# Optimization experiments

Hardware: AMD Instinct MI355X
Metric: run time of the kernel (lower is better)

Reference implementation:

```python
import math
import jax, jax.numpy as jnp
import numpy as np

# gpt-oss config constants (layer_idx=1 -> sliding_window disabled)
HID = 2880
N_HEADS = 64
N_KV = 8
D_HEAD = 64
GROUPS = N_HEADS // N_KV  # 8 query heads per kv head
SLIDING_WINDOW = 0        # layer_idx % 2 == 1 -> full causal attention
SM_SCALE = 1.0 / math.sqrt(D_HEAD)
EPS = 1e-5

ROPE_BASE = 150000.0
INIT_CTX = 4096
SCALING = 32.0
NTK_ALPHA = 1.0
NTK_BETA = 32.0


def _rope_cos_sin(num_tokens: int):
    """YaRN-scaled RoPE tables, fp32, positions 0..num_tokens-1 (offset=0, no cache)."""
    d_half = D_HEAD // 2
    freq = ROPE_BASE ** (np.arange(0, D_HEAD, 2, dtype=np.float64) / D_HEAD)
    concentration = 0.1 * math.log(SCALING) + 1.0
    low = d_half * math.log(INIT_CTX / (NTK_BETA * 2 * math.pi)) / math.log(ROPE_BASE)
    high = d_half * math.log(INIT_CTX / (NTK_ALPHA * 2 * math.pi)) / math.log(ROPE_BASE)
    interpolation = 1.0 / (SCALING * freq)
    extrapolation = 1.0 / freq
    ramp = (np.arange(d_half, dtype=np.float64) - low) / (high - low)
    mask = 1.0 - np.clip(ramp, 0.0, 1.0)
    inv_freq = interpolation * (1.0 - mask) + extrapolation * mask
    t = np.arange(num_tokens, dtype=np.float64)
    freqs = np.outer(t, inv_freq)  # [S, d_half]
    cos = (np.cos(freqs) * concentration).astype(np.float32)
    sin = (np.sin(freqs) * concentration).astype(np.float32)
    return jnp.asarray(cos), jnp.asarray(sin)


def _rotate(x, cos, sin):
    # x: [B, S, nh, D]; cos/sin: [S, D/2]
    c = cos[None, :, None, :]
    s = sin[None, :, None, :]
    x1, x2 = jnp.split(x, 2, axis=-1)
    return jnp.concatenate([x1 * c - x2 * s, x2 * c + x1 * s], axis=-1)


def setup_inputs() -> dict:
    key = jax.random.key(0)
    ks = jax.random.split(key, 5)
    B, S = 1, 1536
    x = jax.random.normal(ks[0], (B, S, HID), dtype=jnp.float32)
    sinks = jax.random.normal(ks[1], (N_HEADS,), dtype=jnp.float32) * 0.5
    norm_scale = jnp.ones((HID,), dtype=jnp.float32)
    qkv_dim = D_HEAD * (N_HEADS + 2 * N_KV)  # 5120
    qkv_w = jax.random.normal(ks[2], (qkv_dim, HID), dtype=jnp.float32) * 0.02
    qkv_b = jnp.zeros((qkv_dim,), dtype=jnp.float32)
    out_w = jax.random.normal(ks[3], (HID, N_HEADS * D_HEAD), dtype=jnp.float32) * 0.02
    out_b = jnp.zeros((HID,), dtype=jnp.float32)
    return {"x": x, "sinks": sinks, "norm_scale": norm_scale,
            "qkv_w": qkv_w, "qkv_b": qkv_b, "out_w": out_w, "out_b": out_b}


def reference(x, sinks, norm_scale, qkv_w, qkv_b, out_w, out_b):
    B, S, _ = x.shape
    # RMSNorm (fp32)
    t = x * jax.lax.rsqrt(jnp.mean(x * x, axis=-1, keepdims=True) + EPS) * norm_scale
    # fused QKV projection
    qkv = jnp.einsum('bsd,od->bso', t, qkv_w) + qkv_b
    q, k, v = jnp.split(qkv, [N_HEADS * D_HEAD, (N_HEADS + N_KV) * D_HEAD], axis=-1)
    q = q.reshape(B, S, N_HEADS, D_HEAD)
    k = k.reshape(B, S, N_KV, D_HEAD)
    v = v.reshape(B, S, N_KV, D_HEAD)
    # RoPE (offset = 0, no cache)
    cos, sin = _rope_cos_sin(S)
    q = _rotate(q, cos, sin)
    k = _rotate(k, cos, sin)
    # GQA: head h = g*N_KV + kv
    q = q.reshape(B, S, GROUPS, N_KV, D_HEAD)
    scores = jnp.einsum('bqgkd,bskd->bgkqs', q, k) * SM_SCALE  # [B,G,KV,S,S]
    i = jnp.arange(S)[:, None]
    j = jnp.arange(S)[None, :]
    allowed = j <= i  # causal
    if SLIDING_WINDOW > 0:
        allowed = allowed & (i - j < SLIDING_WINDOW)
    scores = jnp.where(allowed[None, None, None, :, :], scores, -1e30)
    # softmax with learned per-head sink logit in the denominator
    sink = sinks.reshape(GROUPS, N_KV)[None, :, :, None]  # [1,G,KV,1]
    m = jnp.maximum(jnp.max(scores, axis=-1), sink)       # [B,G,KV,S]
    p = jnp.exp(scores - m[..., None])
    denom = jnp.sum(p, axis=-1) + jnp.exp(sink - m)
    attn = p / denom[..., None]
    o = jnp.einsum('bgkqs,bskd->bqgkd', attn, v).reshape(B, S, N_HEADS * D_HEAD)
    y = jnp.einsum('bse,oe->bso', o, out_w) + out_b
    return x + y
```

## Files before the change

### kernel.cpp

```cpp
#include <hip/hip_runtime.h>
#include <hip/hip_bf16.h>
#include <math.h>

typedef unsigned short u16;
typedef __attribute__((ext_vector_type(8))) short bf16x8;
typedef __attribute__((ext_vector_type(4))) float f32x4;
typedef __attribute__((ext_vector_type(4))) u16 u16x4;
typedef __attribute__((ext_vector_type(8))) u16 u16x8;

#define S_LEN   1536
#define HID     2880
#define NH      64
#define NKV     8
#define DH      64
#define QKV_N   5120
#define QDIM    4096
#define KVDIM   512
#define SMSCALE 0.125f
#define EPSV    1e-5f

__device__ __forceinline__ float b2f(u16 u) {
    unsigned int v = ((unsigned int)u) << 16;
    float f; __builtin_memcpy(&f, &v, 4); return f;
}
__device__ __forceinline__ u16 f2b(float f) {
    __hip_bfloat16 h = __float2bfloat16(f);
    return *reinterpret_cast<u16*>(&h);
}
__device__ __forceinline__ void gld16(const u16* g, u16* l) {
    __builtin_amdgcn_global_load_lds(
        (const __attribute__((address_space(1))) unsigned int*)g,
        (__attribute__((address_space(3))) unsigned int*)l, 16, 0, 0);
}
#define WAIT_VM2()   __builtin_amdgcn_s_waitcnt(0xF72)
#define WAIT_VM0()   __builtin_amdgcn_s_waitcnt(0xF70)
#define WAIT_LGKM0() __builtin_amdgcn_s_waitcnt(0xC07F)

__global__ __launch_bounds__(256) void prep_kernel(
    const float* __restrict__ qkv_w, u16* __restrict__ qkv_w_bf,
    const float* __restrict__ x, const float* __restrict__ ns, u16* __restrict__ t,
    float* __restrict__ cosT, float* __restrict__ sinT,
    const float* __restrict__ out_w, u16* __restrict__ out_w_bf)
{
    __shared__ float red[4];
    const int b = blockIdx.x;
    const int tid = threadIdx.x;
    if (b < 14400) {
        int i = b * 256 + tid;
        float4 v = ((const float4*)qkv_w)[i];
        u16x4 o;
        o.x = f2b(v.x); o.y = f2b(v.y); o.z = f2b(v.z); o.w = f2b(v.w);
        ((u16x4*)qkv_w_bf)[i] = o;
    } else if (b < 15936) {
        const int s = b - 14400;
        const float* xr = x + (size_t)s * HID;
        float ss = 0.f;
        for (int i = tid; i < HID; i += 256) { float v = xr[i]; ss += v * v; }
        for (int off = 32; off > 0; off >>= 1) ss += __shfl_down(ss, off);
        if ((tid & 63) == 0) red[tid >> 6] = ss;
        __syncthreads();
        float tot = red[0] + red[1] + red[2] + red[3];
        float scale = rsqrtf(tot / (float)HID + EPSV);
        u16* tr = t + (size_t)s * HID;
        for (int i = tid; i < HID; i += 256)
            tr[i] = f2b(xr[i] * scale * ns[i]);
    } else if (b < 16128) {
        int idx = (b - 15936) * 256 + tid;
        if (idx >= S_LEN * 32) return;
        int s = idx >> 5, i = idx & 31;
        const double PI2 = 6.283185307179586476925286766559;
        double base = 150000.0;
        double freq = pow(base, (double)(2 * i) / 64.0);
        double conc = 0.1 * log(32.0) + 1.0;
        double low  = 32.0 * log(4096.0 / (32.0 * PI2)) / log(base);
        double high = 32.0 * log(4096.0 / (1.0  * PI2)) / log(base);
        double interp = 1.0 / (32.0 * freq);
        double extrap = 1.0 / freq;
        double ramp = ((double)i - low) / (high - low);
        double msk = 1.0 - fmin(fmax(ramp, 0.0), 1.0);
        double invf = interp * (1.0 - msk) + extrap * msk;
        double ang = (double)s * invf;
        cosT[idx] = (float)(cos(ang) * conc);
        sinT[idx] = (float)(sin(ang) * conc);
    } else {
        int i = (b - 16128) * 256 + tid;
        float4 v = ((const float4*)out_w)[i];
        u16x4 o;
        o.x = f2b(v.x); o.y = f2b(v.y); o.z = f2b(v.z); o.w = f2b(v.w);
        ((u16x4*)out_w_bf)[i] = o;
    }
}

__global__ __launch_bounds__(256) void conv_bf16_kernel(
    const float* __restrict__ src, u16* __restrict__ dst, int n4)
{
    int i = blockIdx.x * 256 + threadIdx.x;
    if (i >= n4) return;
    float4 v = ((const float4*)src)[i];
    u16x4 o;
    o.x = f2b(v.x); o.y = f2b(v.y); o.z = f2b(v.z); o.w = f2b(v.w);
    ((u16x4*)dst)[i] = o;
}

__global__ __launch_bounds__(512, 2) void gemm_bt_8p_kernel(
    const u16* __restrict__ A, const u16* __restrict__ B,
    u16* __restrict__ Cp, u16* __restrict__ Cp2,
    int M, int N, int K, int it0, int it1, int ntm, int ntn)
{
    extern __shared__ __align__(16) u16 smem[];
    u16* sAp = smem;
    u16* sBp = smem + 16384;

    const int tid  = threadIdx.x;
    const int wave = tid >> 6, lane = tid & 63;
    const int quad = lane >> 4, l16 = lane & 15;
    const int wm = wave >> 2, wn = wave & 3;

    const int nwg  = gridDim.x;
    const int cpx  = nwg >> 3;
    const int flat = blockIdx.x;
    const int swz  = (flat & 7) * cpx + (flat >> 3);
    const int tpz  = ntm * ntn;
    const int z    = swz / tpz;
    const int rem  = swz - z * tpz;
    const int nt   = rem / ntm;
    const int mt   = rem - nt * ntm;
    const int bm = mt * 256, bn = nt * 256;
    const int niter = z ? it1 : it0;
    const int kb    = z ? (it0 + (z - 1) * it1) * 32 : 0;
    u16* C = (z < 2) ? (Cp + (size_t)z * M * N) : Cp2;

    const int r2  = tid >> 2;
    const int ks8 = (tid & 3) * 8;
    const u16* gA0 = A + (size_t)(bm + r2) * K + kb + ks8;
    const u16* gA1 = gA0 + (size_t)128 * K;
    int brA = bn + r2;       if (brA > N - 1) brA = N - 1;
    int brB = bn + 128 + r2; if (brB > N - 1) brB = N - 1;
    const u16* gB0 = B + (size_t)brA * K + kb + ks8;
    const u16* gB1 = B + (size_t)brB * K + kb + ks8;
    const int sw = wave * 512;

    f32x4 acc[8][4];
    #pragma unroll
    for (int i = 0; i < 8; i++)
        #pragma unroll
        for (int j = 0; j < 4; j++) acc[i][j] = (f32x4){0.f, 0.f, 0.f, 0.f};

    auto stA = [&](int c, int t) {
        u16* d = sAp + c * 8192;
        const int koff = t * 32;
        gld16(gA0 + koff, d + sw);
        gld16(gA1 + koff, d + 4096 + sw);
    };
    auto stB = [&](int c, int t) {
        u16* d = sBp + c * 8192;
        const int koff = t * 32;
        gld16(gB0 + koff, d + sw);
        gld16(gB1 + koff, d + 4096 + sw);
    };

    bf16x8 bv[4];
    const int arow = wm * 128 + l16;
    const int brow = wn * 64 + l16;
    auto rdB = [&](int c) {
        const u16* p = sBp + c * 8192 + brow * 32 + quad * 8;
        #pragma unroll
        for (int nf = 0; nf < 4; nf++) bv[nf] = *(const bf16x8*)(p + nf * 16 * 32);
    };
    auto mmph = [&](int c, int mh) {
        const u16* p = sAp + c * 8192 + (arow + mh * 64) * 32 + quad * 8;
        bf16x8 av[4];
        #pragma unroll
        for (int mf = 0; mf < 4; mf++) av[mf] = *(const bf16x8*)(p + mf * 16 * 32);
        __builtin_amdgcn_s_setprio(1);
        #pragma unroll
        for (int mf = 0; mf < 4; mf++)
            #pragma unroll
            for (int nf = 0; nf < 4; nf++)
                acc[mh * 4 + mf][nf] = __builtin_amdgcn_mfma_f32_16x16x32_bf16(
                    av[mf], bv[nf], acc[mh * 4 + mf][nf], 0, 0, 0);
        __builtin_amdgcn_s_setprio(0);
    };

    stB(0, 0); stA(0, 0);

    for (int t = 0; t < niter - 1; ++t) {
        const int c = t & 1;
        stB(c ^ 1, t + 1);
        WAIT_VM2();
        __builtin_amdgcn_s_barrier();
        stA(c ^ 1, t + 1);
        rdB(c);
        mmph(c, 0);
        mmph(c, 1);
    }
    {
        const int c = (niter - 1) & 1;
        WAIT_VM0();
        __builtin_amdgcn_s_barrier();
        rdB(c);
        mmph(c, 0);
        mmph(c, 1);
    }

    #pragma unroll
    for (int im = 0; im < 8; im++) {
        const int row0 = bm + wm * 128 + im * 16 + quad * 4;
        #pragma unroll
        for (int nf = 0; nf < 4; nf++) {
            const int col = bn + wn * 64 + nf * 16 + l16;
            if (col < N) {
                #pragma unroll
                for (int r = 0; r < 4; r++)
                    C[(size_t)(row0 + r) * N + col] = f2b(acc[im][nf][r]);
            }
        }
    }
}

__global__ __launch_bounds__(256) void rope_apply_kernel(
    const u16* __restrict__ p0, const u16* __restrict__ p1, const float* __restrict__ bias,
    const float* __restrict__ cosT, const float* __restrict__ sinT,
    u16* __restrict__ q_r, u16* __restrict__ k_r, u16* __restrict__ v_r)
{
    int idx = blockIdx.x * 256 + threadIdx.x;
    if (idx >= S_LEN * 320) return;
    int s = idx / 320;
    int c = idx - s * 320;
    const u16* r0p = p0 + (size_t)s * QKV_N;
    const u16* r1p = p1 + (size_t)s * QKV_N;
    if (c < 288) {
        int hh = c >> 2, j0 = (c & 3) * 8;
        int off = hh * 64;
        u16x8 a1 = *(const u16x8*)(r0p + off + j0);
        u16x8 b1 = *(const u16x8*)(r1p + off + j0);
        u16x8 a2 = *(const u16x8*)(r0p + off + 32 + j0);
        u16x8 b2 = *(const u16x8*)(r1p + off + 32 + j0);
        float bl[8], bh[8], cc[8], sn[8];
        *(float4*)&bl[0] = *(const float4*)(bias + off + j0);
        *(float4*)&bl[4] = *(const float4*)(bias + off + j0 + 4);
        *(float4*)&bh[0] = *(const float4*)(bias + off + 32 + j0);
        *(float4*)&bh[4] = *(const float4*)(bias + off + 32 + j0 + 4);
        *(float4*)&cc[0] = *(const float4*)(cosT + s * 32 + j0);
        *(float4*)&cc[4] = *(const float4*)(cosT + s * 32 + j0 + 4);
        *(float4*)&sn[0] = *(const float4*)(sinT + s * 32 + j0);
        *(float4*)&sn[4] = *(const float4*)(sinT + s * 32 + j0 + 4);
        const float scale = (hh < 64) ? SMSCALE : 1.0f;
        u16x8 lo, hi;
        #pragma unroll
        for (int j = 0; j < 8; j++) {
            float x1 = b2f(a1[j]) + b2f(b1[j]) + bl[j];
            float x2 = b2f(a2[j]) + b2f(b2[j]) + bh[j];
            lo[j] = f2b((x1 * cc[j] - x2 * sn[j]) * scale);
            hi[j] = f2b((x2 * cc[j] + x1 * sn[j]) * scale);
        }
        if (hh < 64) {
            u16* dst = q_r + (size_t)s * QDIM + off;
            *(u16x8*)(dst + j0) = lo;
            *(u16x8*)(dst + 32 + j0) = hi;
        } else {
            u16* dst = k_r + (size_t)s * KVDIM + (hh - 64) * 64;
            *(u16x8*)(dst + j0) = lo;
            *(u16x8*)(dst + 32 + j0) = hi;
        }
    } else {
        int c2 = c - 288;
        int vh = c2 >> 2, i0 = (c2 & 3) * 16;
        int off = QDIM + KVDIM + vh * 64 + i0;
        u16x8 a0 = *(const u16x8*)(r0p + off);
        u16x8 a1 = *(const u16x8*)(r0p + off + 8);
        u16x8 b0 = *(const u16x8*)(r1p + off);
        u16x8 b1 = *(const u16x8*)(r1p + off + 8);
        float bb[16];
        *(float4*)&bb[0]  = *(const float4*)(bias + off);
        *(float4*)&bb[4]  = *(const float4*)(bias + off + 4);
        *(float4*)&bb[8]  = *(const float4*)(bias + off + 8);
        *(float4*)&bb[12] = *(const float4*)(bias + off + 12);
        u16x8 o0, o1;
        #pragma unroll
        for (int j = 0; j < 8; j++) {
            o0[j] = f2b(b2f(a0[j]) + b2f(b0[j]) + bb[j]);
            o1[j] = f2b(b2f(a1[j]) + b2f(b1[j]) + bb[8 + j]);
        }
        u16* dst = v_r + (size_t)s * KVDIM + vh * 64 + i0;
        *(u16x8*)dst = o0;
        *(u16x8*)(dst + 8) = o1;
    }
}

__global__ __launch_bounds__(256) void vt_kernel(
    const u16* __restrict__ v_r, u16* __restrict__ vt)
{
    __shared__ u16 tile[64][72];
    const int s0 = blockIdx.x * 64;
    const int kvh = blockIdx.y;
    const int tid = threadIdx.x;
    const int r = tid >> 3;
    const int c = (tid & 7) * 8;

    #pragma unroll
    for (int rr = 0; rr < 64; rr += 32) {
        uint4 vv = *(const uint4*)(v_r + (size_t)(s0 + r + rr) * KVDIM + kvh * 64 + c);
        const u16* p = (const u16*)&vv;
        #pragma unroll
        for (int j = 0; j < 8; j++) tile[c + j][r + rr] = p[j];
    }
    __syncthreads();
    #pragma unroll
    for (int rr = 0; rr < 64; rr += 32) {
        uint4 ov;
        u16* p = (u16*)&ov;
        #pragma unroll
        for (int j = 0; j < 8; j++) p[j] = tile[r + rr][c + j];
        *(uint4*)(vt + (size_t)(kvh * 64 + r + rr) * S_LEN + s0 + c) = ov;
    }
}

__global__ __launch_bounds__(256) void attn_kernel(
    const u16* __restrict__ q_r, const u16* __restrict__ k_r, const u16* __restrict__ vt,
    const float* __restrict__ sinks, u16* __restrict__ o)
{
    __shared__ __align__(16) u16 sK[2][64 * 72];
    __shared__ __align__(16) u16 sVt[2][64 * 72];
    __shared__ __align__(16) u16 sP[4 * 16 * 72];

    const int bx = blockIdx.x, h = blockIdx.y;
    const int kvh = h & 7;
    const int tid = threadIdx.x, wave = tid >> 6, lane = tid & 63;
    const int quad = lane >> 4, l16 = lane & 15;
    const int srow = tid >> 3;
    const int scol = (tid & 7) * 8;
    u16* sPw = sP + wave * 16 * 72;
    const float sinkv = sinks[h];

    uint4 kreg0, kreg1, vreg0, vreg1;
    const u16* kbase = k_r + (size_t)srow * KVDIM + kvh * 64 + scol;
    const u16* vbase = vt + (size_t)(kvh * 64 + srow) * S_LEN + scol;

    auto issue = [&](int j0) {
        kreg0 = *(const uint4*)(kbase + (size_t)j0 * KVDIM);
        kreg1 = *(const uint4*)(kbase + (size_t)(j0 + 32) * KVDIM);
        vreg0 = *(const uint4*)(vbase + j0);
        vreg1 = *(const uint4*)(vbase + (size_t)32 * S_LEN + j0);
    };
    auto lwrite = [&](int c) {
        *(uint4*)(&sK[c][srow * 72 + scol])        = kreg0;
        *(uint4*)(&sK[c][(srow + 32) * 72 + scol]) = kreg1;
        *(uint4*)(&sVt[c][srow * 72 + scol])        = vreg0;
        *(uint4*)(&sVt[c][(srow + 32) * 72 + scol]) = vreg1;
    };

    for (int phase = 0; phase < 2; ++phase) {
        const int qt = phase ? (23 - bx) : bx;
        const int q_i = qt * 64 + wave * 16 + l16;
        const u16* qp = q_r + (size_t)q_i * QDIM + h * 64 + quad * 8;
        bf16x8 aq0 = *(const bf16x8*)(qp);
        bf16x8 aq1 = *(const bf16x8*)(qp + 32);

        float m_i = sinkv, l_i = 1.0f;
        f32x4 acc[4];
        #pragma unroll
        for (int dt = 0; dt < 4; dt++) acc[dt] = (f32x4){0.f, 0.f, 0.f, 0.f};

        const int ntile = qt + 1;
        issue(0);
        __syncthreads();

        for (int tt = 0; tt < ntile; ++tt) {
            const int c = tt & 1;
            lwrite(c);
            if (tt + 1 < ntile) issue((tt + 1) * 64);
            WAIT_LGKM0();
            __builtin_amdgcn_s_barrier();

            f32x4 sc[4];
            __builtin_amdgcn_s_setprio(1);
            #pragma unroll
            for (int nt = 0; nt < 4; nt++) {
                const u16* kp = &sK[c][(nt * 16 + l16) * 72 + quad * 8];
                bf16x8 bk0 = *(const bf16x8*)(kp);
                bf16x8 bk1 = *(const bf16x8*)(kp + 32);
                f32x4 s0 = (f32x4){0.f, 0.f, 0.f, 0.f};
                s0 = __builtin_amdgcn_mfma_f32_16x16x32_bf16(bk0, aq0, s0, 0, 0, 0);
                s0 = __builtin_amdgcn_mfma_f32_16x16x32_bf16(bk1, aq1, s0, 0, 0, 0);
                sc[nt] = s0;
            }
            __builtin_amdgcn_s_setprio(0);

            if (tt == qt) {
                #pragma unroll
                for (int nt = 0; nt < 4; nt++)
                    #pragma unroll
                    for (int r = 0; r < 4; r++)
                        if (tt * 64 + nt * 16 + quad * 4 + r > q_i) sc[nt][r] = -INFINITY;
            }

            float vmax = sc[0][0];
            #pragma unroll
            for (int nt = 0; nt < 4; nt++)
                #pragma unroll
                for (int r = 0; r < 4; r++) vmax = fmaxf(vmax, sc[nt][r]);
            vmax = fmaxf(vmax, __shfl_xor(vmax, 16));
            vmax = fmaxf(vmax, __shfl_xor(vmax, 32));
            if (__any(vmax > m_i + 8.0f)) {
                float mnew = fmaxf(m_i, vmax);
                float alpha = __expf(m_i - mnew);
                l_i *= alpha;
                #pragma unroll
                for (int dt = 0; dt < 4; dt++)
                    #pragma unroll
                    for (int r = 0; r < 4; r++) acc[dt][r] *= alpha;
                m_i = mnew;
            }
            float ps = 0.f;
            u16x4 pk[4];
            #pragma unroll
            for (int nt = 0; nt < 4; nt++) {
                #pragma unroll
                for (int r = 0; r < 4; r++) {
                    float p = __expf(sc[nt][r] - m_i);
                    ps += p;
                    pk[nt][r] = f2b(p);
                }
            }
            ps += __shfl_xor(ps, 16);
            ps += __shfl_xor(ps, 32);
            l_i += ps;
            #pragma unroll
            for (int nt = 0; nt < 4; nt++)
                *(u16x4*)(sPw + l16 * 72 + nt * 16 + quad * 4) = pk[nt];
            __threadfence_block();

            bf16x8 ap0 = *(const bf16x8*)(sPw + l16 * 72 + quad * 8);
            bf16x8 ap1 = *(const bf16x8*)(sPw + l16 * 72 + 32 + quad * 8);
            __builtin_amdgcn_s_setprio(1);
            #pragma unroll
            for (int dt = 0; dt < 4; dt++) {
                const u16* vp = &sVt[c][(dt * 16 + l16) * 72 + quad * 8];
                bf16x8 bv0 = *(const bf16x8*)(vp);
                bf16x8 bv1 = *(const bf16x8*)(vp + 32);
                acc[dt] = __builtin_amdgcn_mfma_f32_16x16x32_bf16(bv0, ap0, acc[dt], 0, 0, 0);
                acc[dt] = __builtin_amdgcn_mfma_f32_16x16x32_bf16(bv1, ap1, acc[dt], 0, 0, 0);
            }
            __builtin_amdgcn_s_setprio(0);
        }

        float inv = 1.0f / l_i;
        #pragma unroll
        for (int dt = 0; dt < 4; dt++) {
            u16x4 ov;
            #pragma unroll
            for (int r = 0; r < 4; r++) ov[r] = f2b(acc[dt][r] * inv);
            *(u16x4*)(o + (size_t)q_i * QDIM + h * 64 + dt * 16 + quad * 4) = ov;
        }
    }
}

__global__ __launch_bounds__(256) void final_add_kernel(
    const u16* __restrict__ p0, const u16* __restrict__ p1, const u16* __restrict__ p2,
    const float* __restrict__ bias, const float* __restrict__ x, float* __restrict__ out)
{
    int i = blockIdx.x * 256 + threadIdx.x;
    int base = i * 4;
    int col = base % HID;
    float4 xo = *(const float4*)(x + base);
    float4 bi = *(const float4*)(bias + col);
    u16x4 a = ((const u16x4*)p0)[i];
    u16x4 b = ((const u16x4*)p1)[i];
    u16x4 c = ((const u16x4*)p2)[i];
    float4 r;
    r.x = b2f(a.x) + b2f(b.x) + b2f(c.x) + bi.x + xo.x;
    r.y = b2f(a.y) + b2f(b.y) + b2f(c.y) + bi.y + xo.y;
    r.z = b2f(a.z) + b2f(b.z) + b2f(c.z) + bi.z + xo.z;
    r.w = b2f(a.w) + b2f(b.w) + b2f(c.w) + bi.w + xo.w;
    *(float4*)(out + base) = r;
}

extern "C" void kernel_launch(void* const* d_in, const int* in_sizes, int n_in,
                              void* d_out, int out_size, void* d_ws, size_t ws_size,
                              hipStream_t stream)
{
    const float* x          = (const float*)d_in[0];
    const float* sinks      = (const float*)d_in[1];
    const float* norm_scale = (const float*)d_in[2];
    const float* qkv_w      = (const float*)d_in[3];
    const float* qkv_b      = (const float*)d_in[4];
    const float* out_w      = (const float*)d_in[5];
    const float* out_b      = (const float*)d_in[6];
    float* out = (float*)d_out;

    char* ws = (char*)d_ws;
    u16* t        = (u16*)(ws);
    u16* qkv_w_bf = (u16*)(ws + 8847360);
    u16* qkvp0    = (u16*)(ws + 38338560);
    u16* qkvp1    = (u16*)(ws + 54067200);
    float* cosT   = (float*)(ws + 69795840);
    float* sinT   = (float*)(ws + 69992448);
    u16* k_r      = (u16*)(ws);
    u16* vt       = (u16*)(ws + 1572864);
    u16* q_r      = (u16*)(ws + 3145728);
    u16* o        = (u16*)(ws + 15728640);
    u16* v_r      = (u16*)(ws + 28311552);
    u16* outp0    = (u16*)(ws + 28311552);
    u16* outp1    = (u16*)(ws + 37158912);
    u16* outp2    = (u16*)(ws + 3145728);

    const bool fuse_outw = (ws_size >= 93782016ull);
    u16* out_w_bf = fuse_outw ? (u16*)(ws + 70189056) : (u16*)(ws + 46006272);

    static bool lds_attr_set = false;
    if (!lds_attr_set) {
        hipFuncSetAttribute(reinterpret_cast<const void*>(gemm_bt_8p_kernel),
                            hipFuncAttributeMaxDynamicSharedMemorySize, 65536);
        lds_attr_set = true;
    }

    prep_kernel<<<fuse_outw ? 27648 : 16128, 256, 0, stream>>>(
        qkv_w, qkv_w_bf, x, norm_scale, t, cosT, sinT, out_w, out_w_bf);
    gemm_bt_8p_kernel<<<240, 512, 65536, stream>>>(
        t, qkv_w_bf, qkvp0, qkvp0, S_LEN, QKV_N, HID, 45, 45, 6, 20);
    rope_apply_kernel<<<(S_LEN * 320) / 256, 256, 0, stream>>>(
        qkvp0, qkvp1, qkv_b, cosT, sinT, q_r, k_r, v_r);
    vt_kernel<<<dim3(S_LEN / 64, NKV), 256, 0, stream>>>(v_r, vt);
    if (!fuse_outw)
        conv_bf16_kernel<<<(HID * QDIM / 4 + 255) / 256, 256, 0, stream>>>(out_w, out_w_bf, HID * QDIM / 4);
    attn_kernel<<<dim3(12, NH), 256, 0, stream>>>(q_r, k_r, vt, sinks, o);
    gemm_bt_8p_kernel<<<216, 512, 65536, stream>>>(
        o, out_w_bf, outp0, outp2, S_LEN, HID, QDIM, 44, 42, 6, 12);
    final_add_kernel<<<S_LEN * HID / 4 / 256, 256, 0, stream>>>(outp0, outp1, outp2, out_b, x, out);
}
```

Measured before the change: 309.2 us.

## Shrink GEMM N-tile to 128, raise occupancy, add 4-way split-K for out-proj

Halves the GEMM block's N tile from 256 to 128, which cuts LDS use to 48KB and the accumulator set in half. Launch bounds rise to 4 blocks per SM and the grids are roughly doubled. The output projection now uses a 4-way split-K with an extra partial buffer, and the final add sums four partials. The XCD swizzle now handles grid sizes that are not multiples of 8. The pipeline wait is changed to a full vmcnt(0) plus barrier before issuing prefetches, which may reduce load/compute overlap. The smaller tiles also lower operand reuse per block.

```diff
diff --git a/kernel.cpp b/kernel.cpp
--- a/kernel.cpp
+++ b/kernel.cpp
@@ -32,7 +32,6 @@
         (const __attribute__((address_space(1))) unsigned int*)g,
         (__attribute__((address_space(3))) unsigned int*)l, 16, 0, 0);
 }
-#define WAIT_VM2()   __builtin_amdgcn_s_waitcnt(0xF72)
 #define WAIT_VM0()   __builtin_amdgcn_s_waitcnt(0xF70)
 #define WAIT_LGKM0() __builtin_amdgcn_s_waitcnt(0xC07F)
 
@@ -102,9 +101,9 @@
     ((u16x4*)dst)[i] = o;
 }
 
-__global__ __launch_bounds__(512, 2) void gemm_bt_8p_kernel(
+__global__ __launch_bounds__(512, 4) void gemm_bt_8p_kernel(
     const u16* __restrict__ A, const u16* __restrict__ B,
-    u16* __restrict__ Cp, u16* __restrict__ Cp2,
+    u16* __restrict__ Cp, u16* __restrict__ Cp2, u16* __restrict__ Cp3,
     int M, int N, int K, int it0, int it1, int ntm, int ntn)
 {
     extern __shared__ __align__(16) u16 smem[];
@@ -117,34 +116,34 @@
     const int wm = wave >> 2, wn = wave & 3;
 
     const int nwg  = gridDim.x;
-    const int cpx  = nwg >> 3;
+    const int q8   = nwg >> 3, r8 = nwg & 7;
     const int flat = blockIdx.x;
-    const int swz  = (flat & 7) * cpx + (flat >> 3);
+    const int xcd  = flat & 7, loc = flat >> 3;
+    const int swz  = (xcd < r8) ? xcd * (q8 + 1) + loc
+                                : r8 * (q8 + 1) + (xcd - r8) * q8 + loc;
     const int tpz  = ntm * ntn;
     const int z    = swz / tpz;
     const int rem  = swz - z * tpz;
     const int nt   = rem / ntm;
     const int mt   = rem - nt * ntm;
-    const int bm = mt * 256, bn = nt * 256;
+    const int bm = mt * 256, bn = nt * 128;
     const int niter = z ? it1 : it0;
     const int kb    = z ? (it0 + (z - 1) * it1) * 32 : 0;
-    u16* C = (z < 2) ? (Cp + (size_t)z * M * N) : Cp2;
+    u16* C = (z == 0) ? Cp : (z == 1) ? (Cp + (size_t)M * N) : (z == 2) ? Cp2 : Cp3;
 
     const int r2  = tid >> 2;
     const int ks8 = (tid & 3) * 8;
     const u16* gA0 = A + (size_t)(bm + r2) * K + kb + ks8;
     const u16* gA1 = gA0 + (size_t)128 * K;
-    int brA = bn + r2;       if (brA > N - 1) brA = N - 1;
-    int brB = bn + 128 + r2; if (brB > N - 1) brB = N - 1;
+    int brA = bn + r2; if (brA > N - 1) brA = N - 1;
     const u16* gB0 = B + (size_t)brA * K + kb + ks8;
-    const u16* gB1 = B + (size_t)brB * K + kb + ks8;
     const int sw = wave * 512;
 
-    f32x4 acc[8][4];
+    f32x4 acc[8][2];
     #pragma unroll
     for (int i = 0; i < 8; i++)
         #pragma unroll
-        for (int j = 0; j < 4; j++) acc[i][j] = (f32x4){0.f, 0.f, 0.f, 0.f};
+        for (int j = 0; j < 2; j++) acc[i][j] = (f32x4){0.f, 0.f, 0.f, 0.f};
 
     auto stA = [&](int c, int t) {
         u16* d = sAp + c * 8192;
@@ -153,19 +152,17 @@
         gld16(gA1 + koff, d + 4096 + sw);
     };
     auto stB = [&](int c, int t) {
-        u16* d = sBp + c * 8192;
-        const int koff = t * 32;
-        gld16(gB0 + koff, d + sw);
-        gld16(gB1 + koff, d + 4096 + sw);
+        u16* d = sBp + c * 4096;
+        gld16(gB0 + t * 32, d + sw);
     };
 
-    bf16x8 bv[4];
+    bf16x8 bv[2];
     const int arow = wm * 128 + l16;
-    const int brow = wn * 64 + l16;
+    const int brow = wn * 32 + l16;
     auto rdB = [&](int c) {
-        const u16* p = sBp + c * 8192 + brow * 32 + quad * 8;
-        #pragma unroll
-        for (int nf = 0; nf < 4; nf++) bv[nf] = *(const bf16x8*)(p + nf * 16 * 32);
+        const u16* p = sBp + c * 4096 + brow * 32 + quad * 8;
+        #pragma unroll
+        for (int nf = 0; nf < 2; nf++) bv[nf] = *(const bf16x8*)(p + nf * 16 * 32);
     };
     auto mmph = [&](int c, int mh) {
         const u16* p = sAp + c * 8192 + (arow + mh * 64) * 32 + quad * 8;
@@ -176,7 +173,7 @@
         #pragma unroll
         for (int mf = 0; mf < 4; mf++)
             #pragma unroll
-            for (int nf = 0; nf < 4; nf++)
+            for (int nf = 0; nf < 2; nf++)
                 acc[mh * 4 + mf][nf] = __builtin_amdgcn_mfma_f32_16x16x32_bf16(
                     av[mf], bv[nf], acc[mh * 4 + mf][nf], 0, 0, 0);
         __builtin_amdgcn_s_setprio(0);
@@ -186,9 +183,9 @@
 
     for (int t = 0; t < niter - 1; ++t) {
         const int c = t & 1;
+        WAIT_VM0();
+        __builtin_amdgcn_s_barrier();
         stB(c ^ 1, t + 1);
-        WAIT_VM2();
-        __builtin_amdgcn_s_barrier();
         stA(c ^ 1, t + 1);
         rdB(c);
         mmph(c, 0);
@@ -207,8 +204,8 @@
     for (int im = 0; im < 8; im++) {
         const int row0 = bm + wm * 128 + im * 16 + quad * 4;
         #pragma unroll
-        for (int nf = 0; nf < 4; nf++) {
-            const int col = bn + wn * 64 + nf * 16 + l16;
+        for (int nf = 0; nf < 2; nf++) {
+            const int col = bn + wn * 32 + nf * 16 + l16;
             if (col < N) {
                 #pragma unroll
                 for (int r = 0; r < 4; r++)
@@ -458,6 +455,7 @@
 
 __global__ __launch_bounds__(256) void final_add_kernel(
     const u16* __restrict__ p0, const u16* __restrict__ p1, const u16* __restrict__ p2,
+    const u16* __restrict__ p3, int np,
     const float* __restrict__ bias, const float* __restrict__ x, float* __restrict__ out)
 {
     int i = blockIdx.x * 256 + threadIdx.x;
@@ -473,6 +471,10 @@
     r.y = b2f(a.y) + b2f(b.y) + b2f(c.y) + bi.y + xo.y;
     r.z = b2f(a.z) + b2f(b.z) + b2f(c.z) + bi.z + xo.z;
     r.w = b2f(a.w) + b2f(b.w) + b2f(c.w) + bi.w + xo.w;
+    if (np == 4) {
+        u16x4 d = ((const u16x4*)p3)[i];
+        r.x += b2f(d.x); r.y += b2f(d.y); r.z += b2f(d.z); r.w += b2f(d.w);
+    }
     *(float4*)(out + base) = r;
 }
 
@@ -504,6 +506,7 @@
     u16* outp0    = (u16*)(ws + 28311552);
     u16* outp1    = (u16*)(ws + 37158912);
     u16* outp2    = (u16*)(ws + 3145728);
+    u16* outp3    = (u16*)(ws + 46006272);
 
     const bool fuse_outw = (ws_size >= 93782016ull);
     u16* out_w_bf = fuse_outw ? (u16*)(ws + 70189056) : (u16*)(ws + 46006272);
@@ -511,21 +514,29 @@
     static bool lds_attr_set = false;
     if (!lds_attr_set) {
         hipFuncSetAttribute(reinterpret_cast<const void*>(gemm_bt_8p_kernel),
-                            hipFuncAttributeMaxDynamicSharedMemorySize, 65536);
+                            hipFuncAttributeMaxDynamicSharedMemorySize, 49152);
         lds_attr_set = true;
     }
 
     prep_kernel<<<fuse_outw ? 27648 : 16128, 256, 0, stream>>>(
         qkv_w, qkv_w_bf, x, norm_scale, t, cosT, sinT, out_w, out_w_bf);
-    gemm_bt_8p_kernel<<<240, 512, 65536, stream>>>(
-        t, qkv_w_bf, qkvp0, qkvp0, S_LEN, QKV_N, HID, 45, 45, 6, 20);
+    gemm_bt_8p_kernel<<<480, 512, 49152, stream>>>(
+        t, qkv_w_bf, qkvp0, qkvp0, qkvp0, S_LEN, QKV_N, HID, 45, 45, 6, 40);
     rope_apply_kernel<<<(S_LEN * 320) / 256, 256, 0, stream>>>(
         qkvp0, qkvp1, qkv_b, cosT, sinT, q_r, k_r, v_r);
     vt_kernel<<<dim3(S_LEN / 64, NKV), 256, 0, stream>>>(v_r, vt);
     if (!fuse_outw)
         conv_bf16_kernel<<<(HID * QDIM / 4 + 255) / 256, 256, 0, stream>>>(out_w, out_w_bf, HID * QDIM / 4);
     attn_kernel<<<dim3(12, NH), 256, 0, stream>>>(q_r, k_r, vt, sinks, o);
-    gemm_bt_8p_kernel<<<216, 512, 65536, stream>>>(
-        o, out_w_bf, outp0, outp2, S_LEN, HID, QDIM, 44, 42, 6, 12);
-    final_add_kernel<<<S_LEN * HID / 4 / 256, 256, 0, stream>>>(outp0, outp1, outp2, out_b, x, out);
-}
+    if (fuse_outw) {
+        gemm_bt_8p_kernel<<<552, 512, 49152, stream>>>(
+            o, out_w_bf, outp0, outp2, outp3, S_LEN, HID, QDIM, 32, 32, 6, 23);
+        final_add_kernel<<<S_LEN * HID / 4 / 256, 256, 0, stream>>>(
+            outp0, outp1, outp2, outp3, 4, out_b, x, out);
+    } else {
+        gemm_bt_8p_kernel<<<414, 512, 49152, stream>>>(
+            o, out_w_bf, outp0, outp2, outp2, S_LEN, HID, QDIM, 44, 42, 6, 23);
+        final_add_kernel<<<S_LEN * HID / 4 / 256, 256, 0, stream>>>(
+            outp0, outp1, outp2, outp2, 3, out_b, x, out);
+    }
+}
```

Measured after the change: 336.4 us. 8.8% more time.
